# Kernel optimization log

Hardware: AMD Instinct MI355X
Metric: run time of the kernel (lower is better)

Reference implementation:

```python
import jax, jax.numpy as jnp
import numpy as np
import math

NEG = -1e9
B, TX, TY, ODIM = 32, 512, 2048, 80


def setup_inputs() -> dict:
    key = jax.random.key(0)
    k1, k2 = jax.random.split(key)
    return {
        "x_m": jax.random.normal(k1, (B, TX, ODIM), jnp.float32),
        "x_logs": jnp.zeros((B, TX, ODIM), jnp.float32),  # mean_only=True -> zeros_like(x_m)
        "z": jax.random.normal(k2, (B, ODIM, TY), jnp.float32),
        "x_mask": jnp.ones((B, 1, TX), jnp.float32),
        "z_mask": jnp.ones((B, 1, TY), jnp.float32),
    }


def maximum_path(logp, mask, tx_len, ty_len):
    """Monotonic alignment search (Glow-TTS Viterbi DP).
    logp: [B, Tx, Ty] log-likelihoods; mask: [B, Tx, Ty]; lengths: [B] int32.
    Returns hard alignment path [B, Tx, Ty] in {0,1}.
    """
    B_, Tx, Ty = logp.shape
    xs = jnp.arange(Tx)
    logp = jnp.where(mask > 0, logp, NEG)

    # Forward DP over mel frames y: f[x,y] = logp[x,y] + max(f[x-1,y-1], f[x,y-1])
    def fwd_step(prev, y):
        v_cur = jnp.where(xs[None, :] == y, NEG, prev)              # stay (invalid on diagonal)
        prev_shift = jnp.concatenate(
            [jnp.full((B_, 1), NEG, logp.dtype), prev[:, :-1]], axis=1)
        v_prev = jnp.where(xs[None, :] == 0,
                           jnp.where(y == 0, jnp.zeros((), logp.dtype), jnp.asarray(NEG, logp.dtype)),
                           prev_shift)                               # advance
        f = logp[:, :, y] + jnp.maximum(v_prev, v_cur)
        return f, f

    _, fcols = jax.lax.scan(fwd_step, jnp.full((B_, Tx), NEG, logp.dtype), jnp.arange(Ty))
    # fcols: [Ty, B, Tx]

    # Backtrack from (tx_len-1, ty_len-1) down to y=0.
    def bwd_step(index, y):
        active = y < ty_len                                          # [B] bool
        row = jax.nn.one_hot(index, Tx, dtype=logp.dtype) * active[:, None].astype(logp.dtype)
        fm1 = fcols[jnp.maximum(y - 1, 0)]                           # [B, Tx]
        f_here = jnp.take_along_axis(fm1, index[:, None], axis=1)[:, 0]
        f_left = jnp.take_along_axis(fm1, jnp.maximum(index - 1, 0)[:, None], axis=1)[:, 0]
        move = (index != 0) & ((index == y) | (f_here < f_left))
        new_index = jnp.where(active & move, index - 1, index)
        return new_index, row

    _, rows = jax.lax.scan(bwd_step, tx_len - 1, jnp.arange(Ty - 1, -1, -1))
    path = jnp.flip(rows, axis=0).transpose(1, 2, 0)                 # [B, Tx, Ty]
    return path * mask


def reference(x_m, x_logs, z, x_mask, z_mask):
    # attn_mask: [B, Tx, Ty]
    attn_mask = x_mask[:, 0, :, None] * z_mask[:, 0, None, :]

    # Gaussian log-likelihood of each frame z[:, :, y] under each text token's N(x_m, exp(x_logs))
    x_s_sq_r = jnp.exp(-2.0 * x_logs)                                # [B, Tx, D]
    logp1 = jnp.sum(-0.5 * math.log(2.0 * math.pi) - x_logs, axis=2)[:, :, None]
    logp2 = jnp.einsum('btd,bdy->bty', x_s_sq_r, -0.5 * z * z)
    logp3 = jnp.einsum('btd,bdy->bty', x_m * x_s_sq_r, z)
    logp4 = jnp.sum(-0.5 * x_m * x_m * x_s_sq_r, axis=2)[:, :, None]
    logp = logp1 + logp2 + logp3 + logp4                             # [B, Tx, Ty]

    tx_len = jnp.sum(x_mask[:, 0, :], axis=1).astype(jnp.int32)
    ty_len = jnp.sum(z_mask[:, 0, :], axis=1).astype(jnp.int32)
    attn = jax.lax.stop_gradient(
        maximum_path(jax.lax.stop_gradient(logp), attn_mask, tx_len, ty_len))

    # Expand token stats to frame level with the hard alignment.
    z_m = jnp.einsum('bxy,bxd->bdy', attn, x_m)                      # [B, D, Ty]
    z_logs = jnp.einsum('bxy,bxd->bdy', attn, x_logs)                # [B, D, Ty]
    log_durations_ = jnp.log(1e-8 + jnp.sum(attn, axis=-1))[:, None, :] * x_mask  # [B, 1, Tx]
    return z_m, z_logs, log_durations_, attn
```

## Files before the change

### kernel.cpp

```cpp
#include <hip/hip_runtime.h>
#include <math.h>

#define B_ 32
#define TX_ 512
#define TY_ 2048
#define D_ 80
#define NEG (-1e9f)
#define PF 16

__global__ __launch_bounds__(128) void prep_kernel(
    const float* __restrict__ x_m, const float* __restrict__ x_logs,
    float* __restrict__ A1, float* __restrict__ A2, float* __restrict__ Cc,
    int* __restrict__ flag)
{
    int row = blockIdx.x;
    int t = threadIdx.x;
    __shared__ float red[128];
    float contrib = 0.f;
    bool nz = false;
    if (t < D_) {
        float xl = x_logs[(size_t)row * D_ + t];
        float xm = x_m[(size_t)row * D_ + t];
        nz = (xl != 0.f);
        float a1 = expf(-2.f * xl);
        float a2 = xm * a1;
        A1[(size_t)row * D_ + t] = a1;
        A2[(size_t)row * D_ + t] = a2;
        contrib = -0.91893853320467274178f - xl - 0.5f * xm * xm * a1;
    }
    unsigned long long m = __ballot(nz);
    if ((t & 63) == 0 && m) atomicOr(flag, 1);
    red[t] = contrib;
    __syncthreads();
    if (t < 64) {
        float v = red[t] + red[t + 64];
        #pragma unroll
        for (int off = 32; off >= 1; off >>= 1) v += __shfl_down(v, off);
        if (t == 0) Cc[row] = v;
    }
}

__global__ __launch_bounds__(256) void lens_kernel(const float* __restrict__ x_mask,
    const float* __restrict__ z_mask, int* __restrict__ lens)
{
    int blk = blockIdx.x; int t = threadIdx.x;
    __shared__ float red[256];
    float s = 0.f;
    if (blk < B_) {
        for (int i = t; i < TX_; i += 256) s += x_mask[(size_t)blk * TX_ + i];
    } else {
        int b = blk - B_;
        for (int i = t; i < TY_; i += 256) s += z_mask[(size_t)b * TY_ + i];
    }
    red[t] = s; __syncthreads();
    for (int off = 128; off >= 1; off >>= 1) {
        if (t < off) red[t] += red[t + off];
        __syncthreads();
    }
    if (t == 0) lens[blk] = (int)(red[0] + 0.5f);
}

__global__ __launch_bounds__(256) void gemm_zero(
    const int* __restrict__ flag,
    const float* __restrict__ x_m, const float* __restrict__ Cc,
    const float* __restrict__ z,
    const float* __restrict__ x_mask, const float* __restrict__ z_mask,
    float* __restrict__ logpT, int y0, int C)
{
    if (*flag != 0) return;
    __shared__ float xs[D_][136];
    __shared__ float zs[D_][64];
    int b = blockIdx.z;
    int x0 = blockIdx.x * 128;
    int cy0 = blockIdx.y * 64;
    int yy0 = y0 + cy0;
    int tid = threadIdx.x;
    for (int i = tid; i < 128 * D_; i += 256) {
        int m = i / D_, d = i - m * D_;
        xs[d][m] = x_m[((size_t)(b * TX_ + x0 + m)) * D_ + d];
    }
    for (int i = tid; i < D_ * 64; i += 256) {
        int d = i >> 6, n = i & 63;
        zs[d][n] = z[((size_t)(b * D_ + d)) * TY_ + yy0 + n];
    }
    __syncthreads();
    int tm = tid & 15, tn = tid >> 4;
    float acc[8][4];
    float accz[4] = {0.f, 0.f, 0.f, 0.f};
    #pragma unroll
    for (int i = 0; i < 8; ++i)
        #pragma unroll
        for (int j = 0; j < 4; ++j) acc[i][j] = 0.f;
    #pragma unroll 4
    for (int k = 0; k < D_; ++k) {
        float4 a0 = *(const float4*)&xs[k][tm * 8];
        float4 a1v = *(const float4*)&xs[k][tm * 8 + 4];
        float4 zv = *(const float4*)&zs[k][tn * 4];
        float av[8] = {a0.x, a0.y, a0.z, a0.w, a1v.x, a1v.y, a1v.z, a1v.w};
        float zvv[4] = {zv.x, zv.y, zv.z, zv.w};
        #pragma unroll
        for (int j = 0; j < 4; ++j) {
            accz[j] = fmaf(zvv[j], zvv[j], accz[j]);
            #pragma unroll
            for (int i = 0; i < 8; ++i)
                acc[i][j] = fmaf(av[i], zvv[j], acc[i][j]);
        }
    }
    float4 cc0 = *(const float4*)&Cc[(size_t)b * TX_ + x0 + tm * 8];
    float4 cc1 = *(const float4*)&Cc[(size_t)b * TX_ + x0 + tm * 8 + 4];
    float4 xm0 = *(const float4*)&x_mask[(size_t)b * TX_ + x0 + tm * 8];
    float4 xm1 = *(const float4*)&x_mask[(size_t)b * TX_ + x0 + tm * 8 + 4];
    float ccv[8] = {cc0.x, cc0.y, cc0.z, cc0.w, cc1.x, cc1.y, cc1.z, cc1.w};
    float xmv[8] = {xm0.x, xm0.y, xm0.z, xm0.w, xm1.x, xm1.y, xm1.z, xm1.w};
    #pragma unroll
    for (int j = 0; j < 4; ++j) {
        int n = tn * 4 + j;
        float zmv = z_mask[(size_t)b * TY_ + yy0 + n];
        float sz = -0.5f * accz[j];
        float4 o0, o1;
        float* ov0 = (float*)&o0; float* ov1 = (float*)&o1;
        #pragma unroll
        for (int i = 0; i < 4; ++i) {
            float v0 = acc[i][j] + ccv[i] + sz;
            float v1 = acc[i + 4][j] + ccv[i + 4] + sz;
            ov0[i] = (xmv[i] * zmv > 0.f) ? v0 : NEG;
            ov1[i] = (xmv[i + 4] * zmv > 0.f) ? v1 : NEG;
        }
        float* orow = &logpT[((size_t)b * C + cy0 + n) * TX_ + x0 + tm * 8];
        *(float4*)orow = o0;
        *(float4*)(orow + 4) = o1;
    }
}

__global__ __launch_bounds__(256) void gemm_logp(
    const int* __restrict__ flag,
    const float* __restrict__ A1, const float* __restrict__ A2, const float* __restrict__ Cc,
    const float* __restrict__ z, const float* __restrict__ x_mask, const float* __restrict__ z_mask,
    float* __restrict__ logpT, int y0, int C)
{
    if (*flag == 0) return;
    __shared__ float A1s[D_][72];
    __shared__ float A2s[D_][72];
    __shared__ float zs[D_][64];
    int b = blockIdx.z;
    int x0 = blockIdx.x * 64;
    int cy0 = blockIdx.y * 64;
    int yy0 = y0 + cy0;
    int tid = threadIdx.x;
    for (int i = tid; i < 64 * D_; i += 256) {
        int m = i / D_, d = i - m * D_;
        size_t ga = ((size_t)(b * TX_ + x0 + m)) * D_ + d;
        A1s[d][m] = A1[ga];
        A2s[d][m] = A2[ga];
    }
    for (int i = tid; i < D_ * 64; i += 256) {
        int d = i >> 6, n = i & 63;
        zs[d][n] = z[((size_t)(b * D_ + d)) * TY_ + yy0 + n];
    }
    __syncthreads();
    int tm = tid & 15, tn = tid >> 4;
    float acc[4][4];
    #pragma unroll
    for (int i = 0; i < 4; ++i)
        #pragma unroll
        for (int j = 0; j < 4; ++j) acc[i][j] = 0.f;
    #pragma unroll 4
    for (int k = 0; k < D_; ++k) {
        float4 a1 = *(const float4*)&A1s[k][tm * 4];
        float4 a2 = *(const float4*)&A2s[k][tm * 4];
        float4 zv = *(const float4*)&zs[k][tn * 4];
        float av1[4] = {a1.x, a1.y, a1.z, a1.w};
        float av2[4] = {a2.x, a2.y, a2.z, a2.w};
        float zvv[4] = {zv.x, zv.y, zv.z, zv.w};
        #pragma unroll
        for (int j = 0; j < 4; ++j) {
            float h = -0.5f * zvv[j];
            #pragma unroll
            for (int i = 0; i < 4; ++i) {
                float tt = fmaf(h, av1[i], av2[i]);
                acc[i][j] = fmaf(zvv[j], tt, acc[i][j]);
            }
        }
    }
    float4 cc = *(const float4*)&Cc[(size_t)b * TX_ + x0 + tm * 4];
    float4 xm = *(const float4*)&x_mask[(size_t)b * TX_ + x0 + tm * 4];
    float ccv[4] = {cc.x, cc.y, cc.z, cc.w};
    float xmv[4] = {xm.x, xm.y, xm.z, xm.w};
    #pragma unroll
    for (int j = 0; j < 4; ++j) {
        int n = tn * 4 + j;
        float zmv = z_mask[(size_t)b * TY_ + yy0 + n];
        float4 o;
        float* ov = (float*)&o;
        #pragma unroll
        for (int i = 0; i < 4; ++i) {
            float val = acc[i][j] + ccv[i];
            ov[i] = (xmv[i] * zmv > 0.f) ? val : NEG;
        }
        *(float4*)&logpT[((size_t)b * C + cy0 + n) * TX_ + x0 + tm * 4] = o;
    }
}

__device__ __forceinline__ unsigned int dp_stepN_b(int lane, const float4 la, const float4 lb,
    float (&f)[8], unsigned int laneMask)
{
    float lp8[8] = {la.x, la.y, la.z, la.w, lb.x, lb.y, lb.z, lb.w};
    float sh = __shfl_up(f[7], 1);
    float pm0 = (lane == 0) ? NEG : sh;
    unsigned int byt = 0u;
    #pragma unroll
    for (int j = 7; j >= 0; --j) {
        float pm = (j == 0) ? pm0 : f[j - 1];
        byt = byt * 2u + ((f[j] < pm) ? 1u : 0u);
        f[j] = lp8[j] + fmaxf(pm, f[j]);
    }
    return byt & laneMask;
}

__device__ __forceinline__ unsigned int dp_stepD_b(int y, int lane, const float4 la, const float4 lb,
    float (&f)[8], unsigned int laneMask)
{
    float lp8[8] = {la.x, la.y, la.z, la.w, lb.x, lb.y, lb.z, lb.w};
    float sh = __shfl_up(f[7], 1);
    float edge = (y == 0) ? 0.f : NEG;
    float pm0 = (lane == 0) ? edge : sh;
    bool lanehit = (lane == (y >> 3));
    int jeq = y & 7;
    unsigned int byt = 0u;
    #pragma unroll
    for (int j = 7; j >= 0; --j) {
        float pm = (j == 0) ? pm0 : f[j - 1];
        bool ceq = lanehit && (jeq == j);
        byt = byt * 2u + (((f[j] < pm) || ceq) ? 1u : 0u);
        float vc = ceq ? NEG : f[j];
        f[j] = lp8[j] + fmaxf(pm, vc);
    }
    return byt & laneMask;
}

__global__ __launch_bounds__(64) void dp_forward(const float* __restrict__ logpT,
    float* __restrict__ fsave, unsigned char* __restrict__ bits8, int y0, int C)
{
    int b = blockIdx.x, lane = threadIdx.x;
    const float* lp = logpT + (size_t)b * C * TX_ + lane * 8;
    unsigned char* bbase = bits8 + ((size_t)b * TY_ + y0) * 64;
    __shared__ unsigned char sb[16 * 64];
    float f[8];
    if (y0 == 0) {
        #pragma unroll
        for (int j = 0; j < 8; ++j) f[j] = NEG;
    } else {
        float4 fa = *(const float4*)(fsave + (size_t)b * TX_ + lane * 8);
        float4 fb = *(const float4*)(fsave + (size_t)b * TX_ + lane * 8 + 4);
        f[0]=fa.x; f[1]=fa.y; f[2]=fa.z; f[3]=fa.w;
        f[4]=fb.x; f[5]=fb.y; f[6]=fb.z; f[7]=fb.w;
    }
    unsigned int laneMask = (lane == 0) ? 0xFEu : 0xFFu;

    float4 bufA[PF], bufB[PF];
    #pragma unroll
    for (int s = 0; s < PF; ++s) {
        bufA[s] = *(const float4*)(lp + (size_t)s * TX_);
        bufB[s] = *(const float4*)(lp + (size_t)s * TX_ + 4);
    }
    int tD = 0;
    if (y0 < TX_) { tD = TX_ - y0; if (tD > C) tD = C; }
    int t = 0;
    for (; t < tD; t += 16) {
        #pragma unroll
        for (int s = 0; s < 16; ++s) {
            unsigned int byt = dp_stepD_b(y0 + t + s, lane, bufA[s], bufB[s], f, laneMask);
            sb[s * 64 + lane] = (unsigned char)byt;
            int tn = t + s + PF; if (tn >= C) tn = C - 1;
            bufA[s] = *(const float4*)(lp + (size_t)tn * TX_);
            bufB[s] = *(const float4*)(lp + (size_t)tn * TX_ + 4);
        }
        int4 v = ((const int4*)sb)[lane];
        *(int4*)(bbase + (size_t)t * 64 + (size_t)lane * 16) = v;
    }
    for (; t < C; t += 16) {
        #pragma unroll
        for (int s = 0; s < 16; ++s) {
            unsigned int byt = dp_stepN_b(lane, bufA[s], bufB[s], f, laneMask);
            sb[s * 64 + lane] = (unsigned char)byt;
            int tn = t + s + PF; if (tn >= C) tn = C - 1;
            bufA[s] = *(const float4*)(lp + (size_t)tn * TX_);
            bufB[s] = *(const float4*)(lp + (size_t)tn * TX_ + 4);
        }
        int4 v = ((const int4*)sb)[lane];
        *(int4*)(bbase + (size_t)t * 64 + (size_t)lane * 16) = v;
    }
    float4 fa = make_float4(f[0], f[1], f[2], f[3]);
    float4 fb = make_float4(f[4], f[5], f[6], f[7]);
    *(float4*)(fsave + (size_t)b * TX_ + lane * 8) = fa;
    *(float4*)(fsave + (size_t)b * TX_ + lane * 8 + 4) = fb;
}

__global__ __launch_bounds__(64) void backtrack_kernel(
    const unsigned char* __restrict__ bits8, const int* __restrict__ lens,
    const float* __restrict__ x_mask, int* __restrict__ idxA, float* __restrict__ logdur)
{
    int b = blockIdx.x, lane = threadIdx.x;
    __shared__ int durS[TX_];
    for (int x = lane; x < TX_; x += 64) durS[x] = 0;
    int tx_len = lens[b];
    int ty_len = lens[B_ + b];
    int idx = tx_len - 1;
    if (idx < 0) idx = 0;
    int cnt = 0;
    const unsigned long long* bu = (const unsigned long long*)(bits8 + (size_t)b * TY_ * 64);
    for (int w = 0; w < TY_ / 64; ++w) {
        int ytop = TY_ - 1 - w * 64;
        int yl = ytop - lane;
        int Whi = idx >> 6;
        unsigned long long whi = bu[(size_t)yl * 8 + Whi];
        unsigned long long wlo = (Whi > 0) ? bu[(size_t)yl * 8 + Whi - 1] : 0ull;
        int rec = -1;
        for (int s = 0; s < 64; ++s) {
            int y = ytop - s;
            bool active = (y < ty_len);
            if (lane == s) rec = active ? idx : -1;
            if (active) cnt++;
            unsigned long long wsel = ((idx >> 6) == Whi) ? __shfl(whi, s) : __shfl(wlo, s);
            int bit = (int)((wsel >> (idx & 63)) & 1ull);
            if (active && bit) {
                if (lane == 0) durS[idx] = cnt;
                cnt = 0;
                idx -= 1;
            }
        }
        idxA[(size_t)b * TY_ + yl] = rec;
    }
    if (lane == 0) durS[idx] = cnt;
    __syncthreads();
    for (int x = lane; x < TX_; x += 64) {
        float dv = (float)durS[x];
        logdur[(size_t)b * TX_ + x] = logf(1e-8f + dv) * x_mask[(size_t)b * TX_ + x];
    }
}

__global__ __launch_bounds__(256) void attn_write(const int* __restrict__ idxA,
    const float* __restrict__ x_mask, const float* __restrict__ z_mask,
    float* __restrict__ attn_o)
{
    int b = blockIdx.z; int x = blockIdx.y;
    int yq = blockIdx.x * 256 + threadIdx.x;
    int4 iv = ((const int4*)(idxA + (size_t)b * TY_))[yq];
    float xm = x_mask[(size_t)b * TX_ + x];
    float4 zm4 = ((const float4*)(z_mask + (size_t)b * TY_))[yq];
    float4 o;
    o.x = (iv.x == x) ? xm * zm4.x : 0.f;
    o.y = (iv.y == x) ? xm * zm4.y : 0.f;
    o.z = (iv.z == x) ? xm * zm4.z : 0.f;
    o.w = (iv.w == x) ? xm * zm4.w : 0.f;
    ((float4*)(attn_o + ((size_t)(b * TX_ + x)) * TY_))[yq] = o;
}

__global__ __launch_bounds__(256) void zm_write(const int* __restrict__ idxA,
    const float* __restrict__ x_m, const float* __restrict__ x_logs,
    const float* __restrict__ x_mask, const float* __restrict__ z_mask,
    float* __restrict__ z_m_o, float* __restrict__ z_logs_o)
{
    int b = blockIdx.z; int d = blockIdx.y;
    int yq = blockIdx.x * 256 + threadIdx.x;
    int4 iv = ((const int4*)(idxA + (size_t)b * TY_))[yq];
    float4 zm4 = ((const float4*)(z_mask + (size_t)b * TY_))[yq];
    float4 om, ol;
    float* omv = (float*)&om; float* olv = (float*)&ol;
    int ivv[4] = {iv.x, iv.y, iv.z, iv.w};
    float zmv[4] = {zm4.x, zm4.y, zm4.z, zm4.w};
    #pragma unroll
    for (int c = 0; c < 4; ++c) {
        float vm = 0.f, vl = 0.f;
        int ix = ivv[c];
        if (ix >= 0) {
            float wgt = x_mask[(size_t)b * TX_ + ix] * zmv[c];
            size_t ga = ((size_t)(b * TX_ + ix)) * D_ + d;
            vm = wgt * x_m[ga];
            vl = wgt * x_logs[ga];
        }
        omv[c] = vm; olv[c] = vl;
    }
    ((float4*)(z_m_o    + ((size_t)(b * D_ + d)) * TY_))[yq] = om;
    ((float4*)(z_logs_o + ((size_t)(b * D_ + d)) * TY_))[yq] = ol;
}

extern "C" void kernel_launch(void* const* d_in, const int* in_sizes, int n_in,
                              void* d_out, int out_size, void* d_ws, size_t ws_size,
                              hipStream_t stream)
{
    const float* x_m    = (const float*)d_in[0];
    const float* x_logs = (const float*)d_in[1];
    const float* z      = (const float*)d_in[2];
    const float* x_mask = (const float*)d_in[3];
    const float* z_mask = (const float*)d_in[4];
    float* out = (float*)d_out;
    float* z_m_o    = out;
    float* z_logs_o = out + (size_t)B_ * D_ * TY_;
    float* logdur_o = out + (size_t)2 * B_ * D_ * TY_;
    float* attn_o   = logdur_o + (size_t)B_ * TX_;

    char* p = (char*)d_ws;
    float* A1 = (float*)p;            p += (size_t)B_ * TX_ * D_ * 4;
    float* A2 = (float*)p;            p += (size_t)B_ * TX_ * D_ * 4;
    float* Cc = (float*)p;            p += (size_t)B_ * TX_ * 4;
    float* fs = (float*)p;            p += (size_t)B_ * TX_ * 4;
    unsigned char* bits8 = (unsigned char*)p; p += (size_t)B_ * TY_ * 64;
    int* idxA = (int*)p;              p += (size_t)B_ * TY_ * 4;
    int* lens = (int*)p;              p += 256;
    int* flag = (int*)p;              p += 256;
    float* logpC = (float*)p;
    size_t fixed = (size_t)(p - (char*)d_ws);
    size_t avail = (ws_size > fixed) ? (ws_size - fixed) : 0;
    int C = 64;
    const int cands[5] = {2048, 1024, 512, 256, 128};
    for (int i = 0; i < 5; ++i) {
        if ((size_t)B_ * cands[i] * TX_ * 4 <= avail) { C = cands[i]; break; }
    }

    hipMemsetAsync(flag, 0, sizeof(int), stream);
    prep_kernel<<<B_ * TX_, 128, 0, stream>>>(x_m, x_logs, A1, A2, Cc, flag);
    lens_kernel<<<2 * B_, 256, 0, stream>>>(x_mask, z_mask, lens);
    int nc = TY_ / C;
    for (int c = 0; c < nc; ++c) {
        gemm_zero<<<dim3(TX_ / 128, C / 64, B_), 256, 0, stream>>>(
            flag, x_m, Cc, z, x_mask, z_mask, logpC, c * C, C);
        gemm_logp<<<dim3(TX_ / 64, C / 64, B_), 256, 0, stream>>>(
            flag, A1, A2, Cc, z, x_mask, z_mask, logpC, c * C, C);
        dp_forward<<<B_, 64, 0, stream>>>(logpC, fs, bits8, c * C, C);
    }
    backtrack_kernel<<<B_, 64, 0, stream>>>(bits8, lens, x_mask, idxA, logdur_o);
    attn_write<<<dim3(TY_ / 4 / 256, TX_, B_), 256, 0, stream>>>(idxA, x_mask, z_mask, attn_o);
    zm_write<<<dim3(TY_ / 4 / 256, D_, B_), 256, 0, stream>>>(
        idxA, x_m, x_logs, x_mask, z_mask, z_m_o, z_logs_o);
}
```

Baseline: 705.9 us.

## Enlarge zero-logs GEMM tile, drop A1/A2 buffers, direct DP byte stores

```diff
diff --git a/kernel.cpp b/kernel.cpp
--- a/kernel.cpp
+++ b/kernel.cpp
@@ -6,12 +6,13 @@
 #define TY_ 2048
 #define D_ 80
 #define NEG (-1e9f)
-#define PF 16
+#define PF 8
+
+typedef float f32x4 __attribute__((ext_vector_type(4)));
 
 __global__ __launch_bounds__(128) void prep_kernel(
     const float* __restrict__ x_m, const float* __restrict__ x_logs,
-    float* __restrict__ A1, float* __restrict__ A2, float* __restrict__ Cc,
-    int* __restrict__ flag)
+    float* __restrict__ Cc, int* __restrict__ flag)
 {
     int row = blockIdx.x;
     int t = threadIdx.x;
@@ -23,9 +24,6 @@
         float xm = x_m[(size_t)row * D_ + t];
         nz = (xl != 0.f);
         float a1 = expf(-2.f * xl);
-        float a2 = xm * a1;
-        A1[(size_t)row * D_ + t] = a1;
-        A2[(size_t)row * D_ + t] = a2;
         contrib = -0.91893853320467274178f - xl - 0.5f * xm * xm * a1;
     }
     unsigned long long m = __ballot(nz);
@@ -68,73 +66,79 @@
     float* __restrict__ logpT, int y0, int C)
 {
     if (*flag != 0) return;
-    __shared__ float xs[D_][136];
-    __shared__ float zs[D_][64];
+    __shared__ float xs[40][132];
+    __shared__ float zs[40][132];
     int b = blockIdx.z;
     int x0 = blockIdx.x * 128;
-    int cy0 = blockIdx.y * 64;
+    int cy0 = blockIdx.y * 128;
     int yy0 = y0 + cy0;
     int tid = threadIdx.x;
-    for (int i = tid; i < 128 * D_; i += 256) {
-        int m = i / D_, d = i - m * D_;
-        xs[d][m] = x_m[((size_t)(b * TX_ + x0 + m)) * D_ + d];
-    }
-    for (int i = tid; i < D_ * 64; i += 256) {
-        int d = i >> 6, n = i & 63;
-        zs[d][n] = z[((size_t)(b * D_ + d)) * TY_ + yy0 + n];
-    }
-    __syncthreads();
     int tm = tid & 15, tn = tid >> 4;
-    float acc[8][4];
-    float accz[4] = {0.f, 0.f, 0.f, 0.f};
-    #pragma unroll
-    for (int i = 0; i < 8; ++i)
-        #pragma unroll
-        for (int j = 0; j < 4; ++j) acc[i][j] = 0.f;
-    #pragma unroll 4
-    for (int k = 0; k < D_; ++k) {
-        float4 a0 = *(const float4*)&xs[k][tm * 8];
-        float4 a1v = *(const float4*)&xs[k][tm * 8 + 4];
-        float4 zv = *(const float4*)&zs[k][tn * 4];
-        float av[8] = {a0.x, a0.y, a0.z, a0.w, a1v.x, a1v.y, a1v.z, a1v.w};
-        float zvv[4] = {zv.x, zv.y, zv.z, zv.w};
-        #pragma unroll
-        for (int j = 0; j < 4; ++j) {
-            accz[j] = fmaf(zvv[j], zvv[j], accz[j]);
+    float acc[8][8];
+    float accz[8];
+    #pragma unroll
+    for (int i = 0; i < 8; ++i) {
+        accz[i] = 0.f;
+        #pragma unroll
+        for (int j = 0; j < 8; ++j) acc[i][j] = 0.f;
+    }
+
+    for (int h = 0; h < 2; ++h) {
+        if (h) __syncthreads();
+        for (int i = tid; i < 128 * 40; i += 256) {
+            int m = i / 40, d = i - m * 40;
+            xs[d][m] = x_m[((size_t)(b * TX_ + x0 + m)) * D_ + h * 40 + d];
+        }
+        for (int i = tid; i < 40 * 128; i += 256) {
+            int d = i >> 7, n = i & 127;
+            zs[d][n] = z[((size_t)(b * D_ + h * 40 + d)) * TY_ + yy0 + n];
+        }
+        __syncthreads();
+        #pragma unroll 4
+        for (int k = 0; k < 40; ++k) {
+            f32x4 a0 = *(const f32x4*)&xs[k][tm * 4];
+            f32x4 a1 = *(const f32x4*)&xs[k][64 + tm * 4];
+            f32x4 z0 = *(const f32x4*)&zs[k][tn * 4];
+            f32x4 z1 = *(const f32x4*)&zs[k][64 + tn * 4];
+            float av[8], zv[8];
             #pragma unroll
-            for (int i = 0; i < 8; ++i)
-                acc[i][j] = fmaf(av[i], zvv[j], acc[i][j]);
-        }
-    }
-    float4 cc0 = *(const float4*)&Cc[(size_t)b * TX_ + x0 + tm * 8];
-    float4 cc1 = *(const float4*)&Cc[(size_t)b * TX_ + x0 + tm * 8 + 4];
-    float4 xm0 = *(const float4*)&x_mask[(size_t)b * TX_ + x0 + tm * 8];
-    float4 xm1 = *(const float4*)&x_mask[(size_t)b * TX_ + x0 + tm * 8 + 4];
-    float ccv[8] = {cc0.x, cc0.y, cc0.z, cc0.w, cc1.x, cc1.y, cc1.z, cc1.w};
-    float xmv[8] = {xm0.x, xm0.y, xm0.z, xm0.w, xm1.x, xm1.y, xm1.z, xm1.w};
-    #pragma unroll
-    for (int j = 0; j < 4; ++j) {
-        int n = tn * 4 + j;
+            for (int i = 0; i < 4; ++i) { av[i] = a0[i]; av[i+4] = a1[i]; zv[i] = z0[i]; zv[i+4] = z1[i]; }
+            #pragma unroll
+            for (int j = 0; j < 8; ++j) {
+                accz[j] = fmaf(zv[j], zv[j], accz[j]);
+                #pragma unroll
+                for (int i = 0; i < 8; ++i)
+                    acc[i][j] = fmaf(av[i], zv[j], acc[i][j]);
+            }
+        }
+    }
+    f32x4 ccA = *(const f32x4*)&Cc[(size_t)b * TX_ + x0 + tm * 4];
+    f32x4 ccB = *(const f32x4*)&Cc[(size_t)b * TX_ + x0 + 64 + tm * 4];
+    f32x4 xmA = *(const f32x4*)&x_mask[(size_t)b * TX_ + x0 + tm * 4];
+    f32x4 xmB = *(const f32x4*)&x_mask[(size_t)b * TX_ + x0 + 64 + tm * 4];
+    #pragma unroll
+    for (int jj = 0; jj < 8; ++jj) {
+        int n = (jj < 4) ? (tn * 4 + jj) : (64 + tn * 4 + (jj - 4));
         float zmv = z_mask[(size_t)b * TY_ + yy0 + n];
-        float sz = -0.5f * accz[j];
-        float4 o0, o1;
-        float* ov0 = (float*)&o0; float* ov1 = (float*)&o1;
+        float sz = -0.5f * accz[jj];
+        f32x4 oA, oB;
         #pragma unroll
         for (int i = 0; i < 4; ++i) {
-            float v0 = acc[i][j] + ccv[i] + sz;
-            float v1 = acc[i + 4][j] + ccv[i + 4] + sz;
-            ov0[i] = (xmv[i] * zmv > 0.f) ? v0 : NEG;
-            ov1[i] = (xmv[i + 4] * zmv > 0.f) ? v1 : NEG;
-        }
-        float* orow = &logpT[((size_t)b * C + cy0 + n) * TX_ + x0 + tm * 8];
-        *(float4*)orow = o0;
-        *(float4*)(orow + 4) = o1;
+            float vA = acc[i][jj] + ccA[i] + sz;
+            float vB = acc[i + 4][jj] + ccB[i] + sz;
+            oA[i] = (xmA[i] * zmv > 0.f) ? vA : NEG;
+            oB[i] = (xmB[i] * zmv > 0.f) ? vB : NEG;
+        }
+        float* orow = &logpT[((size_t)b * C + cy0 + n) * TX_ + x0];
+        *(f32x4*)(orow + tm * 4) = oA;
+        *(f32x4*)(orow + 64 + tm * 4) = oB;
     }
 }
 
 __global__ __launch_bounds__(256) void gemm_logp(
     const int* __restrict__ flag,
-    const float* __restrict__ A1, const float* __restrict__ A2, const float* __restrict__ Cc,
+    const float* __restrict__ x_m, const float* __restrict__ x_logs,
+    const float* __restrict__ Cc,
     const float* __restrict__ z, const float* __restrict__ x_mask, const float* __restrict__ z_mask,
     float* __restrict__ logpT, int y0, int C)
 {
@@ -150,8 +154,10 @@
     for (int i = tid; i < 64 * D_; i += 256) {
         int m = i / D_, d = i - m * D_;
         size_t ga = ((size_t)(b * TX_ + x0 + m)) * D_ + d;
-        A1s[d][m] = A1[ga];
-        A2s[d][m] = A2[ga];
+        float xl = x_logs[ga], xm = x_m[ga];
+        float a1 = expf(-2.f * xl);
+        A1s[d][m] = a1;
+        A2s[d][m] = xm * a1;
     }
     for (int i = tid; i < D_ * 64; i += 256) {
         int d = i >> 6, n = i & 63;
@@ -166,43 +172,37 @@
         for (int j = 0; j < 4; ++j) acc[i][j] = 0.f;
     #pragma unroll 4
     for (int k = 0; k < D_; ++k) {
-        float4 a1 = *(const float4*)&A1s[k][tm * 4];
-        float4 a2 = *(const float4*)&A2s[k][tm * 4];
-        float4 zv = *(const float4*)&zs[k][tn * 4];
-        float av1[4] = {a1.x, a1.y, a1.z, a1.w};
-        float av2[4] = {a2.x, a2.y, a2.z, a2.w};
-        float zvv[4] = {zv.x, zv.y, zv.z, zv.w};
+        f32x4 a1 = *(const f32x4*)&A1s[k][tm * 4];
+        f32x4 a2 = *(const f32x4*)&A2s[k][tm * 4];
+        f32x4 zv = *(const f32x4*)&zs[k][tn * 4];
         #pragma unroll
         for (int j = 0; j < 4; ++j) {
-            float h = -0.5f * zvv[j];
+            float h = -0.5f * zv[j];
             #pragma unroll
             for (int i = 0; i < 4; ++i) {
-                float tt = fmaf(h, av1[i], av2[i]);
-                acc[i][j] = fmaf(zvv[j], tt, acc[i][j]);
+                float tt = fmaf(h, a1[i], a2[i]);
+                acc[i][j] = fmaf(zv[j], tt, acc[i][j]);
             }
         }
     }
-    float4 cc = *(const float4*)&Cc[(size_t)b * TX_ + x0 + tm * 4];
-    float4 xm = *(const float4*)&x_mask[(size_t)b * TX_ + x0 + tm * 4];
-    float ccv[4] = {cc.x, cc.y, cc.z, cc.w};
-    float xmv[4] = {xm.x, xm.y, xm.z, xm.w};
+    f32x4 cc = *(const f32x4*)&Cc[(size_t)b * TX_ + x0 + tm * 4];
+    f32x4 xm = *(const f32x4*)&x_mask[(size_t)b * TX_ + x0 + tm * 4];
     #pragma unroll
     for (int j = 0; j < 4; ++j) {
         int n = tn * 4 + j;
         float zmv = z_mask[(size_t)b * TY_ + yy0 + n];
-        float4 o;
-        float* ov = (float*)&o;
+        f32x4 o;
         #pragma unroll
         for (int i = 0; i < 4; ++i) {
-            float val = acc[i][j] + ccv[i];
-            ov[i] = (xmv[i] * zmv > 0.f) ? val : NEG;
-        }
-        *(float4*)&logpT[((size_t)b * C + cy0 + n) * TX_ + x0 + tm * 4] = o;
-    }
-}
-
-__device__ __forceinline__ unsigned int dp_stepN_b(int lane, const float4 la, const float4 lb,
-    float (&f)[8], unsigned int laneMask)
+            float val = acc[i][j] + cc[i];
+            o[i] = (xm[i] * zmv > 0.f) ? val : NEG;
+        }
+        *(f32x4*)&logpT[((size_t)b * C + cy0 + n) * TX_ + x0 + tm * 4] = o;
+    }
+}
+
+__device__ __forceinline__ void dp_stepN(int lane, const float4 la, const float4 lb,
+    float (&f)[8], unsigned int laneMask, unsigned char* bpp)
 {
     float lp8[8] = {la.x, la.y, la.z, la.w, lb.x, lb.y, lb.z, lb.w};
     float sh = __shfl_up(f[7], 1);
@@ -214,11 +214,11 @@
         byt = byt * 2u + ((f[j] < pm) ? 1u : 0u);
         f[j] = lp8[j] + fmaxf(pm, f[j]);
     }
-    return byt & laneMask;
-}
-
-__device__ __forceinline__ unsigned int dp_stepD_b(int y, int lane, const float4 la, const float4 lb,
-    float (&f)[8], unsigned int laneMask)
+    *bpp = (unsigned char)(byt & laneMask);
+}
+
+__device__ __forceinline__ void dp_stepD(int y, int lane, const float4 la, const float4 lb,
+    float (&f)[8], unsigned int laneMask, unsigned char* bpp)
 {
     float lp8[8] = {la.x, la.y, la.z, la.w, lb.x, lb.y, lb.z, lb.w};
     float sh = __shfl_up(f[7], 1);
@@ -235,7 +235,7 @@
         float vc = ceq ? NEG : f[j];
         f[j] = lp8[j] + fmaxf(pm, vc);
     }
-    return byt & laneMask;
+    *bpp = (unsigned char)(byt & laneMask);
 }
 
 __global__ __launch_bounds__(64) void dp_forward(const float* __restrict__ logpT,
@@ -243,8 +243,7 @@
 {
     int b = blockIdx.x, lane = threadIdx.x;
     const float* lp = logpT + (size_t)b * C * TX_ + lane * 8;
-    unsigned char* bbase = bits8 + ((size_t)b * TY_ + y0) * 64;
-    __shared__ unsigned char sb[16 * 64];
+    unsigned char* bp = bits8 + ((size_t)b * TY_ + y0) * 64 + lane;
     float f[8];
     if (y0 == 0) {
         #pragma unroll
@@ -266,29 +265,23 @@
     int tD = 0;
     if (y0 < TX_) { tD = TX_ - y0; if (tD > C) tD = C; }
     int t = 0;
-    for (; t < tD; t += 16) {
-        #pragma unroll
-        for (int s = 0; s < 16; ++s) {
-            unsigned int byt = dp_stepD_b(y0 + t + s, lane, bufA[s], bufB[s], f, laneMask);
-            sb[s * 64 + lane] = (unsigned char)byt;
+    for (; t < tD; t += PF) {
+        #pragma unroll
+        for (int s = 0; s < PF; ++s) {
+            dp_stepD(y0 + t + s, lane, bufA[s], bufB[s], f, laneMask, bp + (size_t)(t + s) * 64);
             int tn = t + s + PF; if (tn >= C) tn = C - 1;
             bufA[s] = *(const float4*)(lp + (size_t)tn * TX_);
             bufB[s] = *(const float4*)(lp + (size_t)tn * TX_ + 4);
         }
-        int4 v = ((const int4*)sb)[lane];
-        *(int4*)(bbase + (size_t)t * 64 + (size_t)lane * 16) = v;
-    }
-    for (; t < C; t += 16) {
-        #pragma unroll
-        for (int s = 0; s < 16; ++s) {
-            unsigned int byt = dp_stepN_b(lane, bufA[s], bufB[s], f, laneMask);
-            sb[s * 64 + lane] = (unsigned char)byt;
+    }
+    for (; t < C; t += PF) {
+        #pragma unroll
+        for (int s = 0; s < PF; ++s) {
+            dp_stepN(lane, bufA[s], bufB[s], f, laneMask, bp + (size_t)(t + s) * 64);
             int tn = t + s + PF; if (tn >= C) tn = C - 1;
             bufA[s] = *(const float4*)(lp + (size_t)tn * TX_);
             bufB[s] = *(const float4*)(lp + (size_t)tn * TX_ + 4);
         }
-        int4 v = ((const int4*)sb)[lane];
-        *(int4*)(bbase + (size_t)t * 64 + (size_t)lane * 16) = v;
     }
     float4 fa = make_float4(f[0], f[1], f[2], f[3]);
     float4 fb = make_float4(f[4], f[5], f[6], f[7]);
@@ -401,8 +394,6 @@
     float* attn_o   = logdur_o + (size_t)B_ * TX_;
 
     char* p = (char*)d_ws;
-    float* A1 = (float*)p;            p += (size_t)B_ * TX_ * D_ * 4;
-    float* A2 = (float*)p;            p += (size_t)B_ * TX_ * D_ * 4;
     float* Cc = (float*)p;            p += (size_t)B_ * TX_ * 4;
     float* fs = (float*)p;            p += (size_t)B_ * TX_ * 4;
     unsigned char* bits8 = (unsigned char*)p; p += (size_t)B_ * TY_ * 64;
@@ -412,21 +403,21 @@
     float* logpC = (float*)p;
     size_t fixed = (size_t)(p - (char*)d_ws);
     size_t avail = (ws_size > fixed) ? (ws_size - fixed) : 0;
-    int C = 64;
+    int C = 128;
     const int cands[5] = {2048, 1024, 512, 256, 128};
     for (int i = 0; i < 5; ++i) {
         if ((size_t)B_ * cands[i] * TX_ * 4 <= avail) { C = cands[i]; break; }
     }
 
     hipMemsetAsync(flag, 0, sizeof(int), stream);
-    prep_kernel<<<B_ * TX_, 128, 0, stream>>>(x_m, x_logs, A1, A2, Cc, flag);
+    prep_kernel<<<B_ * TX_, 128, 0, stream>>>(x_m, x_logs, Cc, flag);
     lens_kernel<<<2 * B_, 256, 0, stream>>>(x_mask, z_mask, lens);
     int nc = TY_ / C;
     for (int c = 0; c < nc; ++c) {
-        gemm_zero<<<dim3(TX_ / 128, C / 64, B_), 256, 0, stream>>>(
+        gemm_zero<<<dim3(TX_ / 128, C / 128, B_), 256, 0, stream>>>(
             flag, x_m, Cc, z, x_mask, z_mask, logpC, c * C, C);
         gemm_logp<<<dim3(TX_ / 64, C / 64, B_), 256, 0, stream>>>(
-            flag, A1, A2, Cc, z, x_mask, z_mask, logpC, c * C, C);
+            flag, x_m, x_logs, Cc, z, x_mask, z_mask, logpC, c * C, C);
         dp_forward<<<B_, 64, 0, stream>>>(logpC, fs, bits8, c * C, C);
     }
     backtrack_kernel<<<B_, 64, 0, stream>>>(bits8, lens, x_mask, idxA, logdur_o);
```

After: 673.8 us. -4.6%, faster.
